# Kernel tuning notes

Measured on AMD Instinct MI355X. Metric: run time of the kernel, lower is better.

## Reference

```python
import jax, jax.numpy as jnp
import numpy as np

EMBED_DIM = 1024
NUM_HEADS = 16
HEAD_DIM = EMBED_DIM // NUM_HEADS
SCALE = float(np.sqrt(HEAD_DIM))
B, TQ, TK = 2, 2048, 2048


def setup_inputs() -> dict:
    key = jax.random.key(0)
    ks = jax.random.split(key, 16)
    s = 1.0 / np.sqrt(EMBED_DIM)
    inp = {
        "query": jax.random.normal(ks[0], (B, TQ, EMBED_DIM), jnp.float32),
        "key": jax.random.normal(ks[1], (B, TK, EMBED_DIM), jnp.float32),
        "value": jax.random.normal(ks[2], (B, TK, EMBED_DIM), jnp.float32),
        "key_padding_mask": jnp.zeros((B, TK), dtype=bool),
        "Wq": jax.random.uniform(ks[3], (EMBED_DIM, EMBED_DIM), jnp.float32, -s, s),
        "bq": jax.random.uniform(ks[4], (EMBED_DIM,), jnp.float32, -s, s),
        "Wk": jax.random.uniform(ks[5], (EMBED_DIM, EMBED_DIM), jnp.float32, -s, s),
        "bk": jax.random.uniform(ks[6], (EMBED_DIM,), jnp.float32, -s, s),
        "Wv": jax.random.uniform(ks[7], (EMBED_DIM, EMBED_DIM), jnp.float32, -s, s),
        "bv": jax.random.uniform(ks[8], (EMBED_DIM,), jnp.float32, -s, s),
        "Wo": jax.random.uniform(ks[9], (EMBED_DIM, EMBED_DIM), jnp.float32, -s, s),
        "bo": jax.random.uniform(ks[10], (EMBED_DIM,), jnp.float32, -s, s),
        "clr_bias_q": jax.random.normal(ks[11], (NUM_HEADS, 1, HEAD_DIM), jnp.float32) * 0.02,
        "clr_bias_k": jax.random.normal(ks[12], (NUM_HEADS, 1, HEAD_DIM), jnp.float32) * 0.02,
    }
    return inp


def reference(query, key, value, key_padding_mask, Wq, bq, Wk, bk, Wv, bv, Wo, bo,
              clr_bias_q, clr_bias_k):
    Bsz, Tq, _ = query.shape
    Tk = key.shape[1]

    def split_heads(x, W, b, T):
        # Linear (torch convention: x @ W.T + b) then [B, H, T, Dh]
        y = jnp.einsum('bte,fe->btf', x, W) + b
        return y.reshape(Bsz, T, NUM_HEADS, HEAD_DIM).transpose(0, 2, 1, 3)

    q = split_heads(query, Wq, bq, Tq)   # [B,H,Tq,Dh]
    k = split_heads(key, Wk, bk, Tk)     # [B,H,Tk,Dh]
    v = split_heads(value, Wv, bv, Tk)   # [B,H,Tk,Dh]

    # CLR centering + learned bias (Aitchison similarity)
    q_c = q - jnp.mean(q, axis=-1, keepdims=True) + clr_bias_q[None]
    k_c = k - jnp.mean(k, axis=-1, keepdims=True) + clr_bias_k[None]
    scores = jnp.einsum('bhqd,bhkd->bhqk', q_c, k_c) / SCALE  # [B,H,Tq,Tk]

    mask = key_padding_mask[:, None, None, :]  # [B,1,1,Tk], True = ignore
    scores = jnp.where(mask, -jnp.inf, scores)

    attn = jax.nn.softmax(scores, axis=-1)
    out = jnp.einsum('bhqk,bhkd->bhqd', attn, v)
    out = out.transpose(0, 2, 1, 3).reshape(Bsz, Tq, EMBED_DIM)
    return jnp.einsum('bte,fe->btf', out, Wo) + bo
```

## Files before the change

### kernel.cpp

```cpp
#include <hip/hip_runtime.h>
#include <stdint.h>

static constexpr int EMB   = 1024;
static constexpr int HEADS = 16;
static constexpr int HD    = 64;
static constexpr int BATCH = 2;
static constexpr int SEQ   = 2048;
static constexpr int BT    = BATCH * SEQ;
static constexpr float QSC = 0.18033688011112042f;

typedef short   short8  __attribute__((ext_vector_type(8)));
typedef float   float4v __attribute__((ext_vector_type(4)));

__device__ __forceinline__ ushort f2bf(float f) {
    union { float f; uint32_t i; } v; v.f = f;
    uint32_t x = v.i;
    return (ushort)((x + 0x7FFFu + ((x >> 16) & 1u)) >> 16);
}
__device__ __forceinline__ ushort f2bf_rn(float f) {
    union { float f; uint32_t i; } v; v.f = f;
    return (ushort)((v.i + 0x8000u) >> 16);
}
__device__ __forceinline__ uint32_t pack2bf(float lo, float hi) {
    union { float f; uint32_t u; } a, b; a.f = lo; b.f = hi;
    uint32_t ra = a.u + 0x7FFFu + ((a.u >> 16) & 1u);
    uint32_t rb = b.u + 0x7FFFu + ((b.u >> 16) & 1u);
    return (rb & 0xFFFF0000u) | (ra >> 16);
}
__device__ __forceinline__ float fast_exp2(float x) {
#if __has_builtin(__builtin_amdgcn_exp2f)
    return __builtin_amdgcn_exp2f(x);
#else
    return exp2f(x);
#endif
}

__device__ __forceinline__ void async_ld16(const void* g, void* l) {
    __builtin_amdgcn_global_load_lds(
        (const __attribute__((address_space(1))) void*)g,
        (__attribute__((address_space(3))) void*)l,
        16, 0, 0);
}

__global__ void cvt_all(const float* __restrict__ q, const float* __restrict__ k,
                        const float* __restrict__ v,
                        const float* __restrict__ wq, const float* __restrict__ wk,
                        const float* __restrict__ wv, const float* __restrict__ wo,
                        ushort* __restrict__ qb, ushort* __restrict__ kb,
                        ushort* __restrict__ vb,
                        ushort* __restrict__ wqb, ushort* __restrict__ wkb,
                        ushort* __restrict__ wvb, ushort* __restrict__ wob)
{
    int bid = blockIdx.x;
    const float* src; ushort* dst; size_t off;
    if (bid < 6144) {
        int seg = bid >> 11;
        src = seg == 0 ? q : (seg == 1 ? k : v);
        dst = seg == 0 ? qb : (seg == 1 ? kb : vb);
        off = (size_t)(bid & 2047) * 2048;
    } else {
        int t = bid - 6144, seg = t >> 9;
        src = seg == 0 ? wq : (seg == 1 ? wk : (seg == 2 ? wv : wo));
        dst = seg == 0 ? wqb : (seg == 1 ? wkb : (seg == 2 ? wvb : wob));
        off = (size_t)(t & 511) * 2048;
    }
    size_t base = off + (size_t)threadIdx.x * 8;
    float4 a0 = *(const float4*)(src + base);
    float4 a1 = *(const float4*)(src + base + 4);
    uint32_t o[4] = { pack2bf(a0.x, a0.y), pack2bf(a0.z, a0.w),
                      pack2bf(a1.x, a1.y), pack2bf(a1.z, a1.w) };
    *(uint4*)(dst + base) = *(uint4*)o;
}

__device__ __forceinline__ void gemm_core_128(
    const ushort* __restrict__ A, const ushort* __restrict__ W,
    int m0, int n0, int K,
    ushort* As, ushort* Ws,
    int wid, int lane, float4v acc[4][4])
{
    const int lrow8 = lane >> 3;
    const int gc    = (lane & 7) ^ lrow8;
    const ushort* Ab = A + (size_t)m0 * K + gc * 8;
    const ushort* Wb = W + (size_t)n0 * K + gc * 8;
    const int wm = (wid >> 1) * 64;
    const int wn = (wid & 1) * 64;

    for (int k0 = 0; k0 < K; k0 += 64) {
        __syncthreads();
#pragma unroll
        for (int it = 0; it < 4; ++it) {
            int rg = it * 4 + wid;
            int row = rg * 8 + lrow8;
            async_ld16(Ab + (size_t)row * K + k0, &As[rg * 512]);
            async_ld16(Wb + (size_t)row * K + k0, &Ws[rg * 512]);
        }
        __syncthreads();
#pragma unroll
        for (int ks = 0; ks < 2; ++ks) {
            const int c = ks * 4 + (lane >> 4);
            short8 af[4], wf[4];
#pragma unroll
            for (int i = 0; i < 4; i++) {
                int row = wm + i * 16 + (lane & 15);
                af[i] = *(const short8*)&As[row * 64 + ((c ^ (row & 7)) * 8)];
            }
#pragma unroll
            for (int j = 0; j < 4; j++) {
                int row = wn + j * 16 + (lane & 15);
                wf[j] = *(const short8*)&Ws[row * 64 + ((c ^ (row & 7)) * 8)];
            }
#pragma unroll
            for (int i = 0; i < 4; i++)
#pragma unroll
                for (int j = 0; j < 4; j++)
                    acc[i][j] = __builtin_amdgcn_mfma_f32_16x16x32_bf16(af[i], wf[j], acc[i][j], 0, 0, 0);
        }
    }
}

__global__ __launch_bounds__(256, 3)
void gemm_qkv(const ushort* __restrict__ qb, const ushort* __restrict__ kb,
              const ushort* __restrict__ vb,
              const ushort* __restrict__ wqb, const ushort* __restrict__ wkb,
              const ushort* __restrict__ wvb,
              const float* __restrict__ bq, const float* __restrict__ bk,
              const float* __restrict__ bv,
              const float* __restrict__ cbq, const float* __restrict__ cbk,
              ushort* __restrict__ qc, ushort* __restrict__ kc,
              ushort* __restrict__ vt)
{
    __shared__ __align__(16) ushort As[128 * 64];
    __shared__ __align__(16) ushort Ws[128 * 64];

    const int z = blockIdx.z;
    const ushort* A    = z == 0 ? qb  : (z == 1 ? kb  : vb);
    const ushort* W    = z == 0 ? wqb : (z == 1 ? wkb : wvb);
    const float*  bias = z == 0 ? bq  : (z == 1 ? bk  : bv);
    const float*  clrb = z == 0 ? cbq : cbk;
    const float   scale = z == 0 ? QSC : 1.0f;

    const int tid  = threadIdx.x;
    const int wid  = tid >> 6;
    const int lane = tid & 63;
    const int m0 = blockIdx.y * 128;
    const int n0 = blockIdx.x * 128;
    const int wm = (wid >> 1) * 64;
    const int wn = (wid & 1) * 64;

    float4v acc[4][4];
#pragma unroll
    for (int i = 0; i < 4; i++)
#pragma unroll
        for (int j = 0; j < 4; j++) acc[i][j] = (float4v)0.0f;

    gemm_core_128(A, W, m0, n0, EMB, As, Ws, wid, lane, acc);

    const int h = (n0 + wn) >> 6;
#pragma unroll
    for (int i = 0; i < 4; i++) {
        float ys[4][4];
#pragma unroll
        for (int j = 0; j < 4; j++) {
            float bj = bias[n0 + wn + j * 16 + (lane & 15)];
#pragma unroll
            for (int r = 0; r < 4; r++) ys[j][r] = acc[i][j][r] + bj;
        }
        const int rowb = m0 + wm + i * 16 + ((lane >> 4) << 2);

        if (z < 2) {
            float rs[4];
#pragma unroll
            for (int r = 0; r < 4; r++)
                rs[r] = ys[0][r] + ys[1][r] + ys[2][r] + ys[3][r];
#pragma unroll
            for (int r = 0; r < 4; r++)
#pragma unroll
                for (int off = 1; off < 16; off <<= 1)
                    rs[r] += __shfl_xor(rs[r], off, 64);
            ushort* Yb = z == 0 ? qc : kc;
#pragma unroll
            for (int j = 0; j < 4; j++) {
                int d = j * 16 + (lane & 15);
                float cb = clrb[h * HD + d];
#pragma unroll
                for (int r = 0; r < 4; r++) {
                    int row = rowb + r;
                    int b = row >> 11, t = row & (SEQ - 1);
                    Yb[((size_t)(b * HEADS + h) * SEQ + t) * HD + d] =
                        f2bf((ys[j][r] - rs[r] * (1.0f / 64.0f) + cb) * scale);
                }
            }
        } else {
#pragma unroll
            for (int j = 0; j < 4; j++) {
                int d = j * 16 + (lane & 15);
#pragma unroll
                for (int r = 0; r < 4; r++) {
                    int row = rowb + r;
                    int b = row >> 11, t = row & (SEQ - 1);
                    vt[((size_t)(b * HEADS + h) * HD + d) * SEQ + t] = f2bf(ys[j][r]);
                }
            }
        }
    }
}

__global__ __launch_bounds__(256, 3)
void gemm_out(const ushort* __restrict__ A, const ushort* __restrict__ W,
              const float* __restrict__ bias, float* __restrict__ Y)
{
    __shared__ __align__(16) ushort As[128 * 64];
    __shared__ __align__(16) ushort Ws[128 * 64];

    const int tid  = threadIdx.x;
    const int wid  = tid >> 6;
    const int lane = tid & 63;
    const int m0 = blockIdx.y * 128;
    const int n0 = blockIdx.x * 128;
    const int wm = (wid >> 1) * 64;
    const int wn = (wid & 1) * 64;

    float4v acc[4][4];
#pragma unroll
    for (int i = 0; i < 4; i++)
#pragma unroll
        for (int j = 0; j < 4; j++) acc[i][j] = (float4v)0.0f;

    gemm_core_128(A, W, m0, n0, EMB, As, Ws, wid, lane, acc);

#pragma unroll
    for (int i = 0; i < 4; i++) {
        const int rowb = m0 + wm + i * 16 + ((lane >> 4) << 2);
#pragma unroll
        for (int j = 0; j < 4; j++) {
            int col = n0 + wn + j * 16 + (lane & 15);
            float bj = bias[col];
#pragma unroll
            for (int r = 0; r < 4; r++)
                Y[(size_t)(rowb + r) * EMB + col] = acc[i][j][r] + bj;
        }
    }
}

__global__ __launch_bounds__(256, 3)
void attn_kernel(const ushort* __restrict__ qc,
                 const ushort* __restrict__ kc,
                 const ushort* __restrict__ vt,
                 const unsigned char* __restrict__ mask,
                 ushort* __restrict__ out)
{
    __shared__ __align__(16) ushort Ks[128 * 64];
    __shared__ __align__(16) ushort Vs[64 * 128];
    __shared__ __align__(16) ushort Ps[4][16 * 136];

    const int tid  = threadIdx.x;
    const int wid  = tid >> 6;
    const int lane = tid & 63;

    const int bid = blockIdx.x;
    const int qt = bid & 31;
    const int h  = (bid >> 5) & 15;
    const int b  = bid >> 9;

    const ushort* qbase = qc + ((size_t)(b * HEADS + h)) * SEQ * HD;
    const ushort* kbase = kc + ((size_t)(b * HEADS + h)) * SEQ * HD;
    const ushort* vbase = vt + ((size_t)(b * HEADS + h)) * HD * SEQ;

    const int qrow = qt * 64 + wid * 16 + (lane & 15);
    short8 qf[2];
#pragma unroll
    for (int ks = 0; ks < 2; ++ks)
        qf[ks] = *(const short8*)(qbase + (size_t)qrow * HD + ks * 32 + (lane >> 4) * 8);

    float l_r[4] = {0.f, 0.f, 0.f, 0.f};
    float4v o[4];
#pragma unroll
    for (int j = 0; j < 4; j++) o[j] = (float4v)0.f;

    const int lrow8 = lane >> 3;
    const int gcK   = (lane & 7) ^ lrow8;
    ushort* Pw = &Ps[wid][0];

    for (int kt = 0; kt < SEQ / 128; ++kt) {
        __syncthreads();
#pragma unroll
        for (int it = 0; it < 4; ++it) {
            int row = (it * 4 + wid) * 8 + lrow8;
            async_ld16(kbase + (size_t)(kt * 128 + row) * HD + gcK * 8,
                       &Ks[(it * 4 + wid) * 512]);
        }
#pragma unroll
        for (int it = 0; it < 4; ++it) {
            int row = (it * 4 + wid) * 4 + (lane >> 4);
            int gc  = (lane & 15) ^ (row & 15);
            async_ld16(vbase + (size_t)row * SEQ + kt * 128 + gc * 8,
                       &Vs[(it * 4 + wid) * 512]);
        }
        __syncthreads();

        float4v s[8];
#pragma unroll
        for (int j = 0; j < 8; j++) {
            s[j] = (float4v)0.f;
#pragma unroll
            for (int ks = 0; ks < 2; ks++) {
                int row = j * 16 + (lane & 15);
                int c   = ks * 4 + (lane >> 4);
                short8 kf = *(const short8*)&Ks[row * 64 + ((c ^ (row & 7)) * 8)];
                s[j] = __builtin_amdgcn_mfma_f32_16x16x32_bf16(qf[ks], kf, s[j], 0, 0, 0);
            }
        }

#pragma unroll
        for (int j = 0; j < 8; j++) {
            int key = kt * 128 + j * 16 + (lane & 15);
            float mz = mask[b * SEQ + key] ? -1e30f : 0.0f;
            int prow = ((lane >> 4) << 2) * 136 + j * 16 + (lane & 15);
#pragma unroll
            for (int r = 0; r < 4; r++) {
                float p = fast_exp2(s[j][r] + mz);
                l_r[r] += p;
                Pw[prow + r * 136] = f2bf_rn(p);
            }
        }
        asm volatile("s_waitcnt lgkmcnt(0)" ::: "memory");

        short8 pf[4];
#pragma unroll
        for (int ks = 0; ks < 4; ks++)
            pf[ks] = *(const short8*)&Pw[(lane & 15) * 136 + ks * 32 + (lane >> 4) * 8];

#pragma unroll
        for (int j = 0; j < 4; j++) {
            int d = j * 16 + (lane & 15);
#pragma unroll
            for (int ks = 0; ks < 4; ks++) {
                int c = ks * 4 + (lane >> 4);
                short8 vf = *(const short8*)&Vs[d * 128 + ((c ^ (d & 15)) * 8)];
                o[j] = __builtin_amdgcn_mfma_f32_16x16x32_bf16(pf[ks], vf, o[j], 0, 0, 0);
            }
        }
    }

#pragma unroll
    for (int r = 0; r < 4; r++)
#pragma unroll
        for (int off = 1; off < 16; off <<= 1)
            l_r[r] += __shfl_xor(l_r[r], off, 64);

    const int qrow_out = qt * 64 + wid * 16 + ((lane >> 4) << 2);
#pragma unroll
    for (int j = 0; j < 4; j++) {
        int d = j * 16 + (lane & 15);
#pragma unroll
        for (int r = 0; r < 4; r++) {
            float val = o[j][r] / l_r[r];
            out[((size_t)(b * SEQ + qrow_out + r)) * EMB + h * HD + d] = f2bf(val);
        }
    }
}

extern "C" void kernel_launch(void* const* d_in, const int* in_sizes, int n_in,
                              void* d_out, int out_size, void* d_ws, size_t ws_size,
                              hipStream_t stream)
{
    const float* query = (const float*)d_in[0];
    const float* key_  = (const float*)d_in[1];
    const float* value = (const float*)d_in[2];
    const unsigned char* mask = (const unsigned char*)d_in[3];
    const float* Wq  = (const float*)d_in[4];
    const float* bq  = (const float*)d_in[5];
    const float* Wk  = (const float*)d_in[6];
    const float* bk  = (const float*)d_in[7];
    const float* Wv  = (const float*)d_in[8];
    const float* bv  = (const float*)d_in[9];
    const float* Wo  = (const float*)d_in[10];
    const float* bo  = (const float*)d_in[11];
    const float* cbq = (const float*)d_in[12];
    const float* cbk = (const float*)d_in[13];

    ushort* ws = (ushort*)d_ws;
    const size_t n1 = (size_t)BT * EMB;
    const size_t nw = (size_t)EMB * EMB;
    ushort* qb  = ws;
    ushort* kb  = qb  + n1;
    ushort* vb  = kb  + n1;
    ushort* wqb = vb  + n1;
    ushort* wkb = wqb + nw;
    ushort* wvb = wkb + nw;
    ushort* wob = wvb + nw;
    ushort* qc  = wob + nw;
    ushort* kc  = qc  + n1;
    ushort* vt  = kc  + n1;
    ushort* ao  = qb;

    cvt_all<<<8192, 256, 0, stream>>>(query, key_, value, Wq, Wk, Wv, Wo,
                                      qb, kb, vb, wqb, wkb, wvb, wob);

    dim3 gq(EMB / 128, BT / 128, 3);
    gemm_qkv<<<gq, 256, 0, stream>>>(qb, kb, vb, wqb, wkb, wvb,
                                     bq, bk, bv, cbq, cbk, qc, kc, vt);

    attn_kernel<<<BATCH * HEADS * (SEQ / 64), 256, 0, stream>>>(qc, kc, vt, mask, ao);

    dim3 go(EMB / 128, BT / 128);
    gemm_out<<<go, 256, 0, stream>>>(ao, wob, bo, (float*)d_out);
}
```

Measured before the change: 250.0 us.

## Double query tile per block and prefetch next K/V tile through registers

Each attention block now handles 128 query rows (two 64-row halves) instead of 64, so every K/V tile in shared memory is reused twice and the grid is halved. The next K/V tile is loaded from global memory into registers while the current tile is being computed, then written to shared memory between barriers, replacing the synchronous async-load-then-wait pattern. MFMA sections are also wrapped in s_setprio raises. In exchange, register pressure rises (doubled accumulators, query fragments and prefetch registers) under launch_bounds(256,3), which risks spills or lower occupancy, and there are fewer blocks to spread across CUs.

Result: slower. 280.0 us (+12.0%).

```diff
diff --git a/kernel.cpp b/kernel.cpp
--- a/kernel.cpp
+++ b/kernel.cpp
@@ -258,104 +258,138 @@
     const int lane = tid & 63;
 
     const int bid = blockIdx.x;
-    const int qt = bid & 31;
-    const int h  = (bid >> 5) & 15;
-    const int b  = bid >> 9;
+    const int qt = bid & 15;
+    const int h  = (bid >> 4) & 15;
+    const int b  = bid >> 8;
 
     const ushort* qbase = qc + ((size_t)(b * HEADS + h)) * SEQ * HD;
     const ushort* kbase = kc + ((size_t)(b * HEADS + h)) * SEQ * HD;
     const ushort* vbase = vt + ((size_t)(b * HEADS + h)) * HD * SEQ;
 
-    const int qrow = qt * 64 + wid * 16 + (lane & 15);
-    short8 qf[2];
-#pragma unroll
-    for (int ks = 0; ks < 2; ++ks)
-        qf[ks] = *(const short8*)(qbase + (size_t)qrow * HD + ks * 32 + (lane >> 4) * 8);
-
-    float l_r[4] = {0.f, 0.f, 0.f, 0.f};
-    float4v o[4];
-#pragma unroll
-    for (int j = 0; j < 4; j++) o[j] = (float4v)0.f;
+    short8 qf[2][2];
+#pragma unroll
+    for (int half = 0; half < 2; ++half) {
+        const int qrow = qt * 128 + half * 64 + wid * 16 + (lane & 15);
+#pragma unroll
+        for (int ks = 0; ks < 2; ++ks)
+            qf[half][ks] = *(const short8*)(qbase + (size_t)qrow * HD + ks * 32 + (lane >> 4) * 8);
+    }
+
+    float l_r[2][4];
+    float4v o[2][4];
+#pragma unroll
+    for (int half = 0; half < 2; ++half)
+#pragma unroll
+        for (int j = 0; j < 4; j++) { o[half][j] = (float4v)0.f; l_r[half][j] = 0.f; }
 
     const int lrow8 = lane >> 3;
     const int gcK   = (lane & 7) ^ lrow8;
     ushort* Pw = &Ps[wid][0];
 
+#pragma unroll
+    for (int it = 0; it < 4; ++it) {
+        int rowK = (it * 4 + wid) * 8 + lrow8;
+        async_ld16(kbase + (size_t)rowK * HD + gcK * 8, &Ks[(it * 4 + wid) * 512]);
+        int rowV = (it * 4 + wid) * 4 + (lane >> 4);
+        int gcV  = (lane & 15) ^ (rowV & 15);
+        async_ld16(vbase + (size_t)rowV * SEQ + gcV * 8, &Vs[(it * 4 + wid) * 512]);
+    }
+    __syncthreads();
+
+    uint4 kreg[4], vreg[4];
     for (int kt = 0; kt < SEQ / 128; ++kt) {
-        __syncthreads();
-#pragma unroll
-        for (int it = 0; it < 4; ++it) {
-            int row = (it * 4 + wid) * 8 + lrow8;
-            async_ld16(kbase + (size_t)(kt * 128 + row) * HD + gcK * 8,
-                       &Ks[(it * 4 + wid) * 512]);
-        }
-#pragma unroll
-        for (int it = 0; it < 4; ++it) {
-            int row = (it * 4 + wid) * 4 + (lane >> 4);
-            int gc  = (lane & 15) ^ (row & 15);
-            async_ld16(vbase + (size_t)row * SEQ + kt * 128 + gc * 8,
-                       &Vs[(it * 4 + wid) * 512]);
-        }
-        __syncthreads();
-
-        float4v s[8];
-#pragma unroll
-        for (int j = 0; j < 8; j++) {
-            s[j] = (float4v)0.f;
-#pragma unroll
-            for (int ks = 0; ks < 2; ks++) {
-                int row = j * 16 + (lane & 15);
-                int c   = ks * 4 + (lane >> 4);
-                short8 kf = *(const short8*)&Ks[row * 64 + ((c ^ (row & 7)) * 8)];
-                s[j] = __builtin_amdgcn_mfma_f32_16x16x32_bf16(qf[ks], kf, s[j], 0, 0, 0);
-            }
-        }
-
-#pragma unroll
-        for (int j = 0; j < 8; j++) {
-            int key = kt * 128 + j * 16 + (lane & 15);
-            float mz = mask[b * SEQ + key] ? -1e30f : 0.0f;
-            int prow = ((lane >> 4) << 2) * 136 + j * 16 + (lane & 15);
-#pragma unroll
-            for (int r = 0; r < 4; r++) {
-                float p = fast_exp2(s[j][r] + mz);
-                l_r[r] += p;
-                Pw[prow + r * 136] = f2bf_rn(p);
-            }
-        }
-        asm volatile("s_waitcnt lgkmcnt(0)" ::: "memory");
-
-        short8 pf[4];
-#pragma unroll
-        for (int ks = 0; ks < 4; ks++)
-            pf[ks] = *(const short8*)&Pw[(lane & 15) * 136 + ks * 32 + (lane >> 4) * 8];
-
+        if (kt + 1 < SEQ / 128) {
+#pragma unroll
+            for (int it = 0; it < 4; ++it) {
+                int rowK = (it * 4 + wid) * 8 + lrow8;
+                kreg[it] = *(const uint4*)(kbase + (size_t)((kt + 1) * 128 + rowK) * HD + gcK * 8);
+                int rowV = (it * 4 + wid) * 4 + (lane >> 4);
+                int gcV  = (lane & 15) ^ (rowV & 15);
+                vreg[it] = *(const uint4*)(vbase + (size_t)rowV * SEQ + (kt + 1) * 128 + gcV * 8);
+            }
+        }
+
+        float mzv[8];
+#pragma unroll
+        for (int j = 0; j < 8; ++j)
+            mzv[j] = mask[b * SEQ + kt * 128 + j * 16 + (lane & 15)] ? -1e30f : 0.0f;
+
+#pragma unroll
+        for (int half = 0; half < 2; ++half) {
+            float4v s[8];
+            __builtin_amdgcn_s_setprio(1);
+#pragma unroll
+            for (int j = 0; j < 8; j++) {
+                s[j] = (float4v)0.f;
+#pragma unroll
+                for (int ks = 0; ks < 2; ks++) {
+                    int row = j * 16 + (lane & 15);
+                    int c   = ks * 4 + (lane >> 4);
+                    short8 kf = *(const short8*)&Ks[row * 64 + ((c ^ (row & 7)) * 8)];
+                    s[j] = __builtin_amdgcn_mfma_f32_16x16x32_bf16(qf[half][ks], kf, s[j], 0, 0, 0);
+                }
+            }
+            __builtin_amdgcn_s_setprio(0);
+
+#pragma unroll
+            for (int j = 0; j < 8; j++) {
+                int prow = ((lane >> 4) << 2) * 136 + j * 16 + (lane & 15);
+#pragma unroll
+                for (int r = 0; r < 4; r++) {
+                    float p = fast_exp2(s[j][r] + mzv[j]);
+                    l_r[half][r] += p;
+                    Pw[prow + r * 136] = f2bf_rn(p);
+                }
+            }
+            asm volatile("s_waitcnt lgkmcnt(0)" ::: "memory");
+
+            short8 pf[4];
+#pragma unroll
+            for (int ks = 0; ks < 4; ks++)
+                pf[ks] = *(const short8*)&Pw[(lane & 15) * 136 + ks * 32 + (lane >> 4) * 8];
+
+            __builtin_amdgcn_s_setprio(1);
+#pragma unroll
+            for (int j = 0; j < 4; j++) {
+                int d = j * 16 + (lane & 15);
+#pragma unroll
+                for (int ks = 0; ks < 4; ks++) {
+                    int c = ks * 4 + (lane >> 4);
+                    short8 vf = *(const short8*)&Vs[d * 128 + ((c ^ (d & 15)) * 8)];
+                    o[half][j] = __builtin_amdgcn_mfma_f32_16x16x32_bf16(pf[ks], vf, o[half][j], 0, 0, 0);
+                }
+            }
+            __builtin_amdgcn_s_setprio(0);
+        }
+
+        if (kt + 1 < SEQ / 128) {
+            __syncthreads();
+#pragma unroll
+            for (int it = 0; it < 4; ++it) {
+                *(uint4*)&Ks[(it * 4 + wid) * 512 + lane * 8] = kreg[it];
+                *(uint4*)&Vs[(it * 4 + wid) * 512 + lane * 8] = vreg[it];
+            }
+            __syncthreads();
+        }
+    }
+
+#pragma unroll
+    for (int half = 0; half < 2; ++half) {
+#pragma unroll
+        for (int r = 0; r < 4; r++)
+#pragma unroll
+            for (int off = 1; off < 16; off <<= 1)
+                l_r[half][r] += __shfl_xor(l_r[half][r], off, 64);
+
+        const int qrow_out = qt * 128 + half * 64 + wid * 16 + ((lane >> 4) << 2);
 #pragma unroll
         for (int j = 0; j < 4; j++) {
             int d = j * 16 + (lane & 15);
 #pragma unroll
-            for (int ks = 0; ks < 4; ks++) {
-                int c = ks * 4 + (lane >> 4);
-                short8 vf = *(const short8*)&Vs[d * 128 + ((c ^ (d & 15)) * 8)];
-                o[j] = __builtin_amdgcn_mfma_f32_16x16x32_bf16(pf[ks], vf, o[j], 0, 0, 0);
-            }
-        }
-    }
-
-#pragma unroll
-    for (int r = 0; r < 4; r++)
-#pragma unroll
-        for (int off = 1; off < 16; off <<= 1)
-            l_r[r] += __shfl_xor(l_r[r], off, 64);
-
-    const int qrow_out = qt * 64 + wid * 16 + ((lane >> 4) << 2);
-#pragma unroll
-    for (int j = 0; j < 4; j++) {
-        int d = j * 16 + (lane & 15);
-#pragma unroll
-        for (int r = 0; r < 4; r++) {
-            float val = o[j][r] / l_r[r];
-            out[((size_t)(b * SEQ + qrow_out + r)) * EMB + h * HD + d] = f2bf(val);
+            for (int r = 0; r < 4; r++) {
+                float val = o[half][j][r] / l_r[half][r];
+                out[((size_t)(b * SEQ + qrow_out + r)) * EMB + h * HD + d] = f2bf(val);
+            }
         }
     }
 }
@@ -401,7 +435,7 @@
     gemm_qkv<<<gq, 256, 0, stream>>>(qb, kb, vb, wqb, wkb, wvb,
                                      bq, bk, bv, cbq, cbk, qc, kc, vt);
 
-    attn_kernel<<<BATCH * HEADS * (SEQ / 64), 256, 0, stream>>>(qc, kc, vt, mask, ao);
+    attn_kernel<<<BATCH * HEADS * (SEQ / 128), 256, 0, stream>>>(qc, kc, vt, mask, ao);
 
     dim3 go(EMB / 128, BT / 128);
     gemm_out<<<go, 256, 0, stream>>>(ao, wob, bo, (float*)d_out);
```

## Double-buffer K/V tiles in attention with 64-key tiles and priority hints

Applied to the files above, without the earlier changes.

The attention loop now uses two LDS buffers of 64-key K/V tiles and issues the async load for the next tile before computing on the current one. The goal is to hide global load latency behind the MFMA and exp work, where before the loop did load, sync, then compute. The change also hoists the mask loads and wraps the MFMA sections in s_setprio. In exchange there are twice as many iterations and barriers per block. LDS use per block changes slightly, which can affect occupancy at 3 blocks per CU.

New measurement: 262.6 us. 5.1% more time.

```diff
diff --git a/kernel.cpp b/kernel.cpp
--- a/kernel.cpp
+++ b/kernel.cpp
@@ -249,9 +249,9 @@
                  const unsigned char* __restrict__ mask,
                  ushort* __restrict__ out)
 {
-    __shared__ __align__(16) ushort Ks[128 * 64];
-    __shared__ __align__(16) ushort Vs[64 * 128];
-    __shared__ __align__(16) ushort Ps[4][16 * 136];
+    __shared__ __align__(16) ushort Ks[2][64 * 64];
+    __shared__ __align__(16) ushort Vs[2][64 * 64];
+    __shared__ __align__(16) ushort Ps[4][16 * 72];
 
     const int tid  = threadIdx.x;
     const int wid  = tid >> 6;
@@ -278,69 +278,88 @@
     for (int j = 0; j < 4; j++) o[j] = (float4v)0.f;
 
     const int lrow8 = lane >> 3;
-    const int gcK   = (lane & 7) ^ lrow8;
+    const int gc    = (lane & 7) ^ lrow8;
     ushort* Pw = &Ps[wid][0];
 
-    for (int kt = 0; kt < SEQ / 128; ++kt) {
-        __syncthreads();
-#pragma unroll
-        for (int it = 0; it < 4; ++it) {
-            int row = (it * 4 + wid) * 8 + lrow8;
-            async_ld16(kbase + (size_t)(kt * 128 + row) * HD + gcK * 8,
-                       &Ks[(it * 4 + wid) * 512]);
-        }
-#pragma unroll
-        for (int it = 0; it < 4; ++it) {
-            int row = (it * 4 + wid) * 4 + (lane >> 4);
-            int gc  = (lane & 15) ^ (row & 15);
-            async_ld16(vbase + (size_t)row * SEQ + kt * 128 + gc * 8,
-                       &Vs[(it * 4 + wid) * 512]);
-        }
-        __syncthreads();
-
-        float4v s[8];
-#pragma unroll
-        for (int j = 0; j < 8; j++) {
+#define STAGE(t, sel)                                                          \
+    {                                                                          \
+        _Pragma("unroll")                                                      \
+        for (int it = 0; it < 2; ++it) {                                       \
+            int g   = it * 4 + wid;                                            \
+            int row = g * 8 + lrow8;                                           \
+            async_ld16(kbase + (size_t)((t) * 64 + row) * HD + gc * 8,         \
+                       &Ks[sel][g * 512]);                                     \
+            async_ld16(vbase + (size_t)row * SEQ + (t) * 64 + gc * 8,          \
+                       &Vs[sel][g * 512]);                                     \
+        }                                                                      \
+    }
+
+    STAGE(0, 0);
+    asm volatile("s_waitcnt vmcnt(0)" ::: "memory");
+    __syncthreads();
+
+    int cur = 0;
+    for (int kt = 0; kt < SEQ / 64; ++kt) {
+        if (kt + 1 < SEQ / 64) STAGE(kt + 1, cur ^ 1);
+
+        const ushort* Kc = &Ks[cur][0];
+        const ushort* Vc = &Vs[cur][0];
+
+        float mzv[4];
+#pragma unroll
+        for (int j = 0; j < 4; ++j)
+            mzv[j] = mask[b * SEQ + kt * 64 + j * 16 + (lane & 15)] ? -1e30f : 0.0f;
+
+        float4v s[4];
+        __builtin_amdgcn_s_setprio(1);
+#pragma unroll
+        for (int j = 0; j < 4; j++) {
             s[j] = (float4v)0.f;
 #pragma unroll
             for (int ks = 0; ks < 2; ks++) {
                 int row = j * 16 + (lane & 15);
                 int c   = ks * 4 + (lane >> 4);
-                short8 kf = *(const short8*)&Ks[row * 64 + ((c ^ (row & 7)) * 8)];
+                short8 kf = *(const short8*)&Kc[row * 64 + ((c ^ (row & 7)) * 8)];
                 s[j] = __builtin_amdgcn_mfma_f32_16x16x32_bf16(qf[ks], kf, s[j], 0, 0, 0);
             }
         }
-
-#pragma unroll
-        for (int j = 0; j < 8; j++) {
-            int key = kt * 128 + j * 16 + (lane & 15);
-            float mz = mask[b * SEQ + key] ? -1e30f : 0.0f;
-            int prow = ((lane >> 4) << 2) * 136 + j * 16 + (lane & 15);
+        __builtin_amdgcn_s_setprio(0);
+
+#pragma unroll
+        for (int j = 0; j < 4; j++) {
+            int prow = ((lane >> 4) << 2) * 72 + j * 16 + (lane & 15);
 #pragma unroll
             for (int r = 0; r < 4; r++) {
-                float p = fast_exp2(s[j][r] + mz);
+                float p = fast_exp2(s[j][r] + mzv[j]);
                 l_r[r] += p;
-                Pw[prow + r * 136] = f2bf_rn(p);
+                Pw[prow + r * 72] = f2bf_rn(p);
             }
         }
         asm volatile("s_waitcnt lgkmcnt(0)" ::: "memory");
 
-        short8 pf[4];
-#pragma unroll
-        for (int ks = 0; ks < 4; ks++)
-            pf[ks] = *(const short8*)&Pw[(lane & 15) * 136 + ks * 32 + (lane >> 4) * 8];
-
+        short8 pf[2];
+#pragma unroll
+        for (int ks = 0; ks < 2; ks++)
+            pf[ks] = *(const short8*)&Pw[(lane & 15) * 72 + ks * 32 + (lane >> 4) * 8];
+
+        __builtin_amdgcn_s_setprio(1);
 #pragma unroll
         for (int j = 0; j < 4; j++) {
             int d = j * 16 + (lane & 15);
 #pragma unroll
-            for (int ks = 0; ks < 4; ks++) {
+            for (int ks = 0; ks < 2; ks++) {
                 int c = ks * 4 + (lane >> 4);
-                short8 vf = *(const short8*)&Vs[d * 128 + ((c ^ (d & 15)) * 8)];
+                short8 vf = *(const short8*)&Vc[d * 64 + ((c ^ (d & 7)) * 8)];
                 o[j] = __builtin_amdgcn_mfma_f32_16x16x32_bf16(pf[ks], vf, o[j], 0, 0, 0);
             }
         }
-    }
+        __builtin_amdgcn_s_setprio(0);
+
+        asm volatile("s_waitcnt vmcnt(0)" ::: "memory");
+        __syncthreads();
+        cur ^= 1;
+    }
+#undef STAGE
 
 #pragma unroll
     for (int r = 0; r < 4; r++)
```
